# Optimization experiments

Measured on AMD Instinct MI355X. Metric: run time of the kernel, lower is better.

The kernel has to match this reference:

```python
import jax, jax.numpy as jnp
import numpy as np
from jax import lax

WINDOW_SIZE = 11
C1 = 0.01 ** 2
C2 = 0.03 ** 2


def make_window(window_size: int) -> jnp.ndarray:
    # scipy.ndimage.gaussian_filter(np.ones(ws), sigma) with mode='reflect'
    # preserves constant inputs exactly, so gauss_1d == ones(ws).
    # outer(ones, ones) / sum -> uniform box window of weight 1/ws^2.
    return jnp.full((window_size, window_size), 1.0 / (window_size * window_size), dtype=jnp.float32)


def setup_inputs() -> dict:
    key = jax.random.key(0)
    k1, k2 = jax.random.split(key)
    B, C, D, H, W = 1, 1, 64, 512, 512
    x = jax.random.uniform(k1, (B, C, D, H, W), dtype=jnp.float32)
    y = jax.random.uniform(k2, (B, C, D, H, W), dtype=jnp.float32)
    window = make_window(WINDOW_SIZE)
    return {"x": x, "y": y, "window": window}


def _windowed_sum(imgs, window):
    # imgs: [N,1,H,W]; window: [ws,ws]. 'same' cross-correlation (window is symmetric).
    ws = window.shape[0]
    pad = ws // 2
    w = window[None, None, :, :]  # [O=1, I=1, ws, ws]
    return lax.conv_general_dilated(
        imgs, w, window_strides=(1, 1), padding=[(pad, pad), (pad, pad)],
        dimension_numbers=("NCHW", "OIHW", "NCHW"))


def reference(x, y, window):
    B, C, D, H, W = x.shape
    # Fold depth into the conv batch dim: every depth slice is an independent 2D SSIM.
    xs = x.transpose(0, 2, 1, 3, 4).reshape(B * D, C, H, W)
    ys = y.transpose(0, 2, 1, 3, 4).reshape(B * D, C, H, W)
    # Single batched conv over [x, y, x^2, y^2, x*y]
    stacked = jnp.concatenate([xs, ys, xs * xs, ys * ys, xs * ys], axis=0)
    conv = _windowed_sum(stacked, window)
    mu_x, mu_y, e_x2, e_y2, e_xy = jnp.split(conv, 5, axis=0)
    mu_x_sq = mu_x * mu_x
    mu_y_sq = mu_y * mu_y
    mu_xy = mu_x * mu_y
    sigma_x_sq = e_x2 - mu_x_sq
    sigma_y_sq = e_y2 - mu_y_sq
    sigma_xy = e_xy - mu_xy
    ssim_map = ((2.0 * mu_xy + C1) * (2.0 * sigma_xy + C2)) / (
        (mu_x_sq + mu_y_sq + C1) * (sigma_x_sq + sigma_y_sq + C2))
    # Per-slice means averaged over slices == global mean (all slices same size).
    return 1.0 - ssim_map.mean()
```

## Files before the change

kernel.cpp:

```cpp
#include <hip/hip_runtime.h>


constexpr int IMG   = 512;
constexpr int RB    = 16;
constexpr int BANDS = IMG / RB;
constexpr int WPB   = 4;
constexpr int NBLK  = 64 * BANDS / WPB;
constexpr float K1 = 1.4641f;
constexpr float K2 = 13.1769f;

__device__ __forceinline__ float shr1(float v) {
  return __int_as_float(__builtin_amdgcn_update_dpp(
      0, __float_as_int(v), 0x138, 0xF, 0xF, true));
}
__device__ __forceinline__ float shl1(float v) {
  return __int_as_float(__builtin_amdgcn_update_dpp(
      0, __float_as_int(v), 0x130, 0xF, 0xF, true));
}

template <bool ATOMIC>
__global__ __launch_bounds__(256, 2) void ssim_main(const float* __restrict__ x,
                                                    const float* __restrict__ y,
                                                    float* __restrict__ out_ws) {
  __shared__ float wsum[WPB];

  const int tid  = threadIdx.x;
  const int lane = tid & 63;
  const int wid  = tid >> 6;

  const int bid  = blockIdx.x;
  const int xcd  = bid & 7;
  const int qq   = bid >> 3;
  const int z    = xcd * 8 + (qq >> 3);
  const int band = (qq & 7) * WPB + wid;
  const int o0   = band * RB;
  const int gs   = o0 - 5;

  const float* xs = x + (size_t)z * IMG * IMG + lane * 8;
  const float* ys = y + (size_t)z * IMG * IMG + lane * 8;

  float sX[8] = {}, sY[8] = {}, sXX[8] = {}, sYY[8] = {}, sXY[8] = {};
  float cxA[8], cyA[8], oxA[8], oyA[8];
  float cxB[8], cyB[8], oxB[8], oyB[8];
  float mcA = 0.f, mcB = 0.f, moA = 1.f, moB = 1.f;
  float acc = 0.f;

  auto LDraw = [&](int gr, float (&dx)[8], float (&dy)[8]) -> float {
    const int grc = gr < 0 ? 0 : (gr > IMG - 1 ? IMG - 1 : gr);
    const float* px = xs + (size_t)grc * IMG;
    const float* py = ys + (size_t)grc * IMG;
    const float4 a = *(const float4*)px;
    const float4 b = *(const float4*)(px + 4);
    const float4 c = *(const float4*)py;
    const float4 d = *(const float4*)(py + 4);
    dx[0] = a.x; dx[1] = a.y; dx[2] = a.z; dx[3] = a.w;
    dx[4] = b.x; dx[5] = b.y; dx[6] = b.z; dx[7] = b.w;
    dy[0] = c.x; dy[1] = c.y; dy[2] = c.z; dy[3] = c.w;
    dy[4] = d.x; dy[5] = d.y; dy[6] = d.z; dy[7] = d.w;
    return ((unsigned)gr < (unsigned)IMG) ? 1.f : 0.f;
  };

  auto consumeW = [&](const float (&cx)[8], const float (&cy)[8], float mc) {
#pragma unroll
    for (int j = 0; j < 8; ++j) {
      const float cxm = cx[j] * mc, cym = cy[j] * mc;
      sX[j] += cxm;
      sY[j] += cym;
      sXX[j] = fmaf(cx[j], cxm, sXX[j]);
      sYY[j] = fmaf(cy[j], cym, sYY[j]);
      sXY[j] = fmaf(cx[j], cym, sXY[j]);
    }
  };

  auto consumeS = [&](const float (&cx)[8], const float (&cy)[8], float mc,
                      const float (&ox)[8], const float (&oy)[8], float mo) {
#pragma unroll
    for (int j = 0; j < 8; ++j) {
      const float cxm = cx[j] * mc, cym = cy[j] * mc;
      const float oxm = ox[j] * mo, oym = oy[j] * mo;
      sX[j] += cxm - oxm;
      sY[j] += cym - oym;
      sXX[j] = fmaf(cx[j], cxm, fmaf(-ox[j], oxm, sXX[j]));
      sYY[j] = fmaf(cy[j], cym, fmaf(-oy[j], oym, sYY[j]));
      sXY[j] = fmaf(cx[j], cym, fmaf(-ox[j], oym, sXY[j]));
    }
  };

  auto hwin = [&](const float (&S)[8], float (&B)[8]) {
    const float vm5  = shr1(S[3]);
    const float vm4  = shr1(S[4]);
    const float vm3  = shr1(S[5]);
    const float vm2  = shr1(S[6]);
    const float vm1  = shr1(S[7]);
    const float vp8  = shl1(S[0]);
    const float vp9  = shl1(S[1]);
    const float vp10 = shl1(S[2]);
    const float vp11 = shl1(S[3]);
    const float vp12 = shl1(S[4]);
    float s = (((vm5 + vm4) + (vm3 + vm2)) + ((vm1 + S[0]) + (S[1] + S[2]))) +
              ((S[3] + S[4]) + S[5]);
    B[0] = s;
    s += S[6]  - vm5;  B[1] = s;
    s += S[7]  - vm4;  B[2] = s;
    s += vp8   - vm3;  B[3] = s;
    s += vp9   - vm2;  B[4] = s;
    s += vp10  - vm1;  B[5] = s;
    s += vp11  - S[0]; B[6] = s;
    s += vp12  - S[1]; B[7] = s;
  };

  auto outp = [&]() {
    float bX[8], bY[8], bXX[8], bYY[8], bXY[8];
    hwin(sX, bX); hwin(sY, bY); hwin(sXX, bXX); hwin(sYY, bYY); hwin(sXY, bXY);
#pragma unroll
    for (int j = 0; j < 8; ++j) {
      const float bx  = bX[j];
      const float by  = bY[j];
      const float bxy = bx * by;
      const float sq  = fmaf(bx, bx, by * by);
      const float n1  = fmaf(2.f, bxy, K1);
      const float n2  = fmaf(242.f, bXY[j], fmaf(-2.f, bxy, K2));
      const float d1  = sq + K1;
      const float d2  = fmaf(121.f, bXX[j] + bYY[j], K2 - sq);
      acc += (n1 * n2) * __builtin_amdgcn_rcpf(d1 * d2);
    }
  };

  mcA = LDraw(gs, cxA, cyA);
#pragma unroll
  for (int j = 0; j < 8; ++j) {
    oxA[j] = 0.f; oyA[j] = 0.f; oxB[j] = 0.f; oyB[j] = 0.f;
  }

#pragma unroll 1
  for (int i = 0; i < 10; i += 2) {
    mcB = LDraw(gs + i + 1, cxB, cyB);
    __builtin_amdgcn_sched_barrier(0);
    consumeW(cxA, cyA, mcA);
    mcA = LDraw(gs + i + 2, cxA, cyA);
    __builtin_amdgcn_sched_barrier(0);
    consumeW(cxB, cyB, mcB);
  }

#pragma unroll 1
  for (int i = 10; i < RB + 10; i += 2) {
    mcB = LDraw(gs + i + 1, cxB, cyB);
    moB = LDraw(gs + i - 10, oxB, oyB);
    __builtin_amdgcn_sched_barrier(0);
    consumeS(cxA, cyA, mcA, oxA, oyA, moA);
    outp();
    mcA = LDraw(gs + i + 2, cxA, cyA);
    moA = LDraw(gs + i - 9, oxA, oyA);
    __builtin_amdgcn_sched_barrier(0);
    consumeS(cxB, cyB, mcB, oxB, oyB, moB);
    outp();
  }

#pragma unroll
  for (int off = 32; off > 0; off >>= 1) acc += __shfl_down(acc, off, 64);
  if (lane == 0) wsum[wid] = acc;
  __syncthreads();
  if (tid == 0) {
    const float t = wsum[0] + wsum[1] + wsum[2] + wsum[3];
    if (ATOMIC) {
      atomicAdd(out_ws, t);
    } else {
      out_ws[bid] = t;
    }
  }
}

__global__ void ssim_finalize(const float* __restrict__ partials, int n,
                              float* __restrict__ out) {
  __shared__ float wsum[4];
  float acc = 0.f;
  for (int i = threadIdx.x; i < n; i += 256) acc += partials[i];
#pragma unroll
  for (int off = 32; off > 0; off >>= 1) acc += __shfl_down(acc, off, 64);
  if ((threadIdx.x & 63) == 0) wsum[threadIdx.x >> 6] = acc;
  __syncthreads();
  if (threadIdx.x == 0) {
    const float t = wsum[0] + wsum[1] + wsum[2] + wsum[3];
    out[0] = 1.0f - t * (1.0f / (64.0f * 512.0f * 512.0f));
  }
}

__global__ void ssim_zero(float* p) {
  if (threadIdx.x == 0) p[0] = 0.f;
}

__global__ void ssim_finalize_atomic(const float* __restrict__ accp,
                                     float* __restrict__ out) {
  if (threadIdx.x == 0)
    out[0] = 1.0f - accp[0] * (1.0f / (64.0f * 512.0f * 512.0f));
}

extern "C" void kernel_launch(void* const* d_in, const int* in_sizes, int n_in,
                              void* d_out, int out_size, void* d_ws, size_t ws_size,
                              hipStream_t stream) {
  const float* x = (const float*)d_in[0];
  const float* y = (const float*)d_in[1];
  float* out = (float*)d_out;

  dim3 grid(NBLK);
  dim3 block(256);

  if (ws_size >= (size_t)NBLK * sizeof(float)) {
    float* partials = (float*)d_ws;
    ssim_main<false><<<grid, block, 0, stream>>>(x, y, partials);
    ssim_finalize<<<1, 256, 0, stream>>>(partials, NBLK, out);
  } else {
    float* accp = (float*)d_ws;
    ssim_zero<<<1, 64, 0, stream>>>(accp);
    ssim_main<true><<<grid, block, 0, stream>>>(x, y, accp);
    ssim_finalize_atomic<<<1, 64, 0, stream>>>(accp, out);
  }
}
```

Measured before the change: 172.0 us.

## Stream rows into an LDS ring via async global_load_lds with one-wave blocks

Each block is now a single wavefront handling one 16-row band. Input rows (both the incoming and the outgoing row of the sliding window) are fetched with asynchronous global-to-LDS loads into a three-slot ring, and explicit vmcnt waits keep two rows in flight ahead of the computation. The goal is to hide global-load latency and free the registers that were used for the double-buffered rows. In exchange the kernel takes a 24KB LDS footprint per block, depends on hand-counted waitcnt values, and launches four times as many smaller blocks.

```diff
diff --git a/kernel.cpp b/kernel.cpp
--- a/kernel.cpp
+++ b/kernel.cpp
@@ -4,8 +4,7 @@
 constexpr int IMG   = 512;
 constexpr int RB    = 16;
 constexpr int BANDS = IMG / RB;
-constexpr int WPB   = 4;
-constexpr int NBLK  = 64 * BANDS / WPB;
+constexpr int NBLK  = 64 * BANDS;
 constexpr float K1 = 1.4641f;
 constexpr float K2 = 13.1769f;
 
@@ -18,72 +17,61 @@
       0, __float_as_int(v), 0x130, 0xF, 0xF, true));
 }
 
+__device__ __forceinline__ void gl16(const float* g, float* l) {
+  __builtin_amdgcn_global_load_lds(
+      (const __attribute__((address_space(1))) void*)g,
+      (__attribute__((address_space(3))) void*)l, 16, 0, 0);
+}
+
+#define VW(n) do {                                                             \
+    asm volatile("s_waitcnt vmcnt(%0)" :: "n"(n) : "memory");                  \
+    __builtin_amdgcn_sched_barrier(0);                                         \
+  } while (0)
+
 template <bool ATOMIC>
-__global__ __launch_bounds__(256, 2) void ssim_main(const float* __restrict__ x,
-                                                    const float* __restrict__ y,
-                                                    float* __restrict__ out_ws) {
-  __shared__ float wsum[WPB];
-
-  const int tid  = threadIdx.x;
-  const int lane = tid & 63;
-  const int wid  = tid >> 6;
-
+__global__ __launch_bounds__(64, 1) void ssim_main(const float* __restrict__ x,
+                                                   const float* __restrict__ y,
+                                                   float* __restrict__ out_ws) {
+  __shared__ float ring[3 * 2048];
+
+  const int lane = threadIdx.x;
   const int bid  = blockIdx.x;
   const int xcd  = bid & 7;
   const int qq   = bid >> 3;
-  const int z    = xcd * 8 + (qq >> 3);
-  const int band = (qq & 7) * WPB + wid;
+  const int z    = xcd * 8 + (qq >> 5);
+  const int band = qq & 31;
   const int o0   = band * RB;
   const int gs   = o0 - 5;
 
-  const float* xs = x + (size_t)z * IMG * IMG + lane * 8;
-  const float* ys = y + (size_t)z * IMG * IMG + lane * 8;
+  const float* xs = x + (size_t)z * IMG * IMG;
+  const float* ys = y + (size_t)z * IMG * IMG;
+  const int l4 = lane * 4;
+  const int lw = lane * 8;
 
   float sX[8] = {}, sY[8] = {}, sXX[8] = {}, sYY[8] = {}, sXY[8] = {};
-  float cxA[8], cyA[8], oxA[8], oyA[8];
-  float cxB[8], cyB[8], oxB[8], oyB[8];
-  float mcA = 0.f, mcB = 0.f, moA = 1.f, moB = 1.f;
   float acc = 0.f;
 
-  auto LDraw = [&](int gr, float (&dx)[8], float (&dy)[8]) -> float {
+  auto issue_c = [&](int slot) {
+    const int gr  = gs + slot;
     const int grc = gr < 0 ? 0 : (gr > IMG - 1 ? IMG - 1 : gr);
-    const float* px = xs + (size_t)grc * IMG;
-    const float* py = ys + (size_t)grc * IMG;
-    const float4 a = *(const float4*)px;
-    const float4 b = *(const float4*)(px + 4);
-    const float4 c = *(const float4*)py;
-    const float4 d = *(const float4*)(py + 4);
-    dx[0] = a.x; dx[1] = a.y; dx[2] = a.z; dx[3] = a.w;
-    dx[4] = b.x; dx[5] = b.y; dx[6] = b.z; dx[7] = b.w;
-    dy[0] = c.x; dy[1] = c.y; dy[2] = c.z; dy[3] = c.w;
-    dy[4] = d.x; dy[5] = d.y; dy[6] = d.z; dy[7] = d.w;
-    return ((unsigned)gr < (unsigned)IMG) ? 1.f : 0.f;
-  };
-
-  auto consumeW = [&](const float (&cx)[8], const float (&cy)[8], float mc) {
-#pragma unroll
-    for (int j = 0; j < 8; ++j) {
-      const float cxm = cx[j] * mc, cym = cy[j] * mc;
-      sX[j] += cxm;
-      sY[j] += cym;
-      sXX[j] = fmaf(cx[j], cxm, sXX[j]);
-      sYY[j] = fmaf(cy[j], cym, sYY[j]);
-      sXY[j] = fmaf(cx[j], cym, sXY[j]);
-    }
-  };
-
-  auto consumeS = [&](const float (&cx)[8], const float (&cy)[8], float mc,
-                      const float (&ox)[8], const float (&oy)[8], float mo) {
-#pragma unroll
-    for (int j = 0; j < 8; ++j) {
-      const float cxm = cx[j] * mc, cym = cy[j] * mc;
-      const float oxm = ox[j] * mo, oym = oy[j] * mo;
-      sX[j] += cxm - oxm;
-      sY[j] += cym - oym;
-      sXX[j] = fmaf(cx[j], cxm, fmaf(-ox[j], oxm, sXX[j]));
-      sYY[j] = fmaf(cy[j], cym, fmaf(-oy[j], oym, sYY[j]));
-      sXY[j] = fmaf(cx[j], cym, fmaf(-ox[j], oym, sXY[j]));
-    }
+    const int rb  = (slot % 3) * 2048;
+    const float* gx = xs + grc * IMG + l4;
+    const float* gy = ys + grc * IMG + l4;
+    gl16(gx,       &ring[rb]);
+    gl16(gx + 256, &ring[rb + 256]);
+    gl16(gy,       &ring[rb + 512]);
+    gl16(gy + 256, &ring[rb + 768]);
+  };
+  auto issue_o = [&](int slot) {
+    const int gr  = gs + slot - 11;
+    const int grc = gr < 0 ? 0 : (gr > IMG - 1 ? IMG - 1 : gr);
+    const int rb  = (slot % 3) * 2048;
+    const float* gx = xs + grc * IMG + l4;
+    const float* gy = ys + grc * IMG + l4;
+    gl16(gx,       &ring[rb + 1024]);
+    gl16(gx + 256, &ring[rb + 1280]);
+    gl16(gy,       &ring[rb + 1536]);
+    gl16(gy + 256, &ring[rb + 1792]);
   };
 
   auto hwin = [&](const float (&S)[8], float (&B)[8]) {
@@ -126,46 +114,88 @@
     }
   };
 
-  mcA = LDraw(gs, cxA, cyA);
-#pragma unroll
-  for (int j = 0; j < 8; ++j) {
-    oxA[j] = 0.f; oyA[j] = 0.f; oxB[j] = 0.f; oyB[j] = 0.f;
-  }
-
+  auto consumeW = [&](int slot) {
+    const int rb = (slot % 3) * 2048;
+    const float mc = ((unsigned)(gs + slot) < (unsigned)IMG) ? 1.f : 0.f;
+    const float4 a = *(const float4*)&ring[rb + lw];
+    const float4 b = *(const float4*)&ring[rb + lw + 4];
+    const float4 c = *(const float4*)&ring[rb + 512 + lw];
+    const float4 d = *(const float4*)&ring[rb + 512 + lw + 4];
+    const float cx[8] = {a.x, a.y, a.z, a.w, b.x, b.y, b.z, b.w};
+    const float cy[8] = {c.x, c.y, c.z, c.w, d.x, d.y, d.z, d.w};
+#pragma unroll
+    for (int j = 0; j < 8; ++j) {
+      const float cxm = cx[j] * mc, cym = cy[j] * mc;
+      sX[j] += cxm;
+      sY[j] += cym;
+      sXX[j] = fmaf(cx[j], cxm, sXX[j]);
+      sYY[j] = fmaf(cy[j], cym, sYY[j]);
+      sXY[j] = fmaf(cx[j], cym, sXY[j]);
+    }
+  };
+
+  auto consumeS = [&](int slot) {
+    const int rb = (slot % 3) * 2048;
+    const float mc = ((unsigned)(gs + slot) < (unsigned)IMG) ? 1.f : 0.f;
+    const float mo = (slot >= 11 && (gs + slot - 11) >= 0) ? 1.f : 0.f;
+    const float4 a = *(const float4*)&ring[rb + lw];
+    const float4 b = *(const float4*)&ring[rb + lw + 4];
+    const float4 c = *(const float4*)&ring[rb + 512 + lw];
+    const float4 d = *(const float4*)&ring[rb + 512 + lw + 4];
+    const float4 e = *(const float4*)&ring[rb + 1024 + lw];
+    const float4 f = *(const float4*)&ring[rb + 1024 + lw + 4];
+    const float4 g = *(const float4*)&ring[rb + 1536 + lw];
+    const float4 h = *(const float4*)&ring[rb + 1536 + lw + 4];
+    const float cx[8] = {a.x, a.y, a.z, a.w, b.x, b.y, b.z, b.w};
+    const float cy[8] = {c.x, c.y, c.z, c.w, d.x, d.y, d.z, d.w};
+    const float ox[8] = {e.x, e.y, e.z, e.w, f.x, f.y, f.z, f.w};
+    const float oy[8] = {g.x, g.y, g.z, g.w, h.x, h.y, h.z, h.w};
+#pragma unroll
+    for (int j = 0; j < 8; ++j) {
+      const float cxm = cx[j] * mc, cym = cy[j] * mc;
+      const float oxm = ox[j] * mo, oym = oy[j] * mo;
+      sX[j] += cxm - oxm;
+      sY[j] += cym - oym;
+      sXX[j] = fmaf(cx[j], cxm, fmaf(-ox[j], oxm, sXX[j]));
+      sYY[j] = fmaf(cy[j], cym, fmaf(-oy[j], oym, sYY[j]));
+      sXY[j] = fmaf(cx[j], cym, fmaf(-ox[j], oym, sXY[j]));
+    }
+    outp();
+  };
+
+  issue_c(0);
+  issue_c(1);
 #pragma unroll 1
-  for (int i = 0; i < 10; i += 2) {
-    mcB = LDraw(gs + i + 1, cxB, cyB);
-    __builtin_amdgcn_sched_barrier(0);
-    consumeW(cxA, cyA, mcA);
-    mcA = LDraw(gs + i + 2, cxA, cyA);
-    __builtin_amdgcn_sched_barrier(0);
-    consumeW(cxB, cyB, mcB);
-  }
-
+  for (int s = 0; s < 10; ++s) {
+    issue_c(s + 2);
+    VW(8);
+    consumeW(s);
+  }
+  issue_o(10);
+  issue_o(11);
+  issue_c(12);
+  issue_o(12);
+  VW(12);
+  consumeS(10);
 #pragma unroll 1
-  for (int i = 10; i < RB + 10; i += 2) {
-    mcB = LDraw(gs + i + 1, cxB, cyB);
-    moB = LDraw(gs + i - 10, oxB, oyB);
-    __builtin_amdgcn_sched_barrier(0);
-    consumeS(cxA, cyA, mcA, oxA, oyA, moA);
-    outp();
-    mcA = LDraw(gs + i + 2, cxA, cyA);
-    moA = LDraw(gs + i - 9, oxA, oyA);
-    __builtin_amdgcn_sched_barrier(0);
-    consumeS(cxB, cyB, mcB, oxB, oyB, moB);
-    outp();
-  }
+  for (int s = 11; s <= 23; ++s) {
+    issue_c(s + 2);
+    issue_o(s + 2);
+    VW(16);
+    consumeS(s);
+  }
+  VW(8);
+  consumeS(24);
+  VW(0);
+  consumeS(25);
 
 #pragma unroll
   for (int off = 32; off > 0; off >>= 1) acc += __shfl_down(acc, off, 64);
-  if (lane == 0) wsum[wid] = acc;
-  __syncthreads();
-  if (tid == 0) {
-    const float t = wsum[0] + wsum[1] + wsum[2] + wsum[3];
+  if (lane == 0) {
     if (ATOMIC) {
-      atomicAdd(out_ws, t);
+      atomicAdd(out_ws, acc);
     } else {
-      out_ws[bid] = t;
+      out_ws[bid] = acc;
     }
   }
 }
@@ -203,7 +233,7 @@
   float* out = (float*)d_out;
 
   dim3 grid(NBLK);
-  dim3 block(256);
+  dim3 block(64);
 
   if (ws_size >= (size_t)NBLK * sizeof(float)) {
     float* partials = (float*)d_ws;
```

After: 191.1 us. +11.1%, slower.

## Share row loads across warps via LDS ring with async global-to-LDS copies

Applied to the files above, without the earlier changes.

Each block now covers a 64-row group. Its four waves take overlapping 26-row windows of that group (16 output rows plus a 10-row halo) from a 16-slot LDS ring buffer that is filled with global_load_lds, one wave issuing each row four rows ahead. Before, every wave read its own halo rows and its outgoing rows straight from global memory, so global traffic was about 2.6x the image. Now each row is fetched once per block, and the rows leaving the window are re-read from LDS. The cost is a block-wide barrier on every row step and serialized staggering: each wave sits idle for the steps outside its window, which lowers compute utilization.

```diff
diff --git a/kernel.cpp b/kernel.cpp
--- a/kernel.cpp
+++ b/kernel.cpp
@@ -2,10 +2,10 @@
 
 
 constexpr int IMG   = 512;
-constexpr int RB    = 16;
-constexpr int BANDS = IMG / RB;
-constexpr int WPB   = 4;
-constexpr int NBLK  = 64 * BANDS / WPB;
+constexpr int GRB   = 64;
+constexpr int NROW  = GRB + 10;
+constexpr int NBLK  = 64 * (IMG / GRB);
+constexpr int SLOTS = 16;
 constexpr float K1 = 1.4641f;
 constexpr float K2 = 13.1769f;
 
@@ -16,13 +16,20 @@
 __device__ __forceinline__ float shl1(float v) {
   return __int_as_float(__builtin_amdgcn_update_dpp(
       0, __float_as_int(v), 0x130, 0xF, 0xF, true));
+}
+
+__device__ __forceinline__ void gl16(const float* g, float* l) {
+  __builtin_amdgcn_global_load_lds(
+      (const __attribute__((address_space(1))) void*)g,
+      (__attribute__((address_space(3))) void*)l, 16, 0, 0);
 }
 
 template <bool ATOMIC>
 __global__ __launch_bounds__(256, 2) void ssim_main(const float* __restrict__ x,
                                                     const float* __restrict__ y,
                                                     float* __restrict__ out_ws) {
-  __shared__ float wsum[WPB];
+  __shared__ float ring[SLOTS * 1024];
+  __shared__ float wsum[4];
 
   const int tid  = threadIdx.x;
   const int lane = tid & 63;
@@ -32,58 +39,27 @@
   const int xcd  = bid & 7;
   const int qq   = bid >> 3;
   const int z    = xcd * 8 + (qq >> 3);
-  const int band = (qq & 7) * WPB + wid;
-  const int o0   = band * RB;
-  const int gs   = o0 - 5;
-
-  const float* xs = x + (size_t)z * IMG * IMG + lane * 8;
-  const float* ys = y + (size_t)z * IMG * IMG + lane * 8;
+  const int g    = qq & 7;
+  const int R0   = g * GRB - 5;
+
+  const float* xs = x + (size_t)z * IMG * IMG;
+  const float* ys = y + (size_t)z * IMG * IMG;
+  const int l4 = lane * 4;
+  const int lw = lane * 8;
 
   float sX[8] = {}, sY[8] = {}, sXX[8] = {}, sYY[8] = {}, sXY[8] = {};
-  float cxA[8], cyA[8], oxA[8], oyA[8];
-  float cxB[8], cyB[8], oxB[8], oyB[8];
-  float mcA = 0.f, mcB = 0.f, moA = 1.f, moB = 1.f;
   float acc = 0.f;
 
-  auto LDraw = [&](int gr, float (&dx)[8], float (&dy)[8]) -> float {
-    const int grc = gr < 0 ? 0 : (gr > IMG - 1 ? IMG - 1 : gr);
-    const float* px = xs + (size_t)grc * IMG;
-    const float* py = ys + (size_t)grc * IMG;
-    const float4 a = *(const float4*)px;
-    const float4 b = *(const float4*)(px + 4);
-    const float4 c = *(const float4*)py;
-    const float4 d = *(const float4*)(py + 4);
-    dx[0] = a.x; dx[1] = a.y; dx[2] = a.z; dx[3] = a.w;
-    dx[4] = b.x; dx[5] = b.y; dx[6] = b.z; dx[7] = b.w;
-    dy[0] = c.x; dy[1] = c.y; dy[2] = c.z; dy[3] = c.w;
-    dy[4] = d.x; dy[5] = d.y; dy[6] = d.z; dy[7] = d.w;
-    return ((unsigned)gr < (unsigned)IMG) ? 1.f : 0.f;
-  };
-
-  auto consumeW = [&](const float (&cx)[8], const float (&cy)[8], float mc) {
-#pragma unroll
-    for (int j = 0; j < 8; ++j) {
-      const float cxm = cx[j] * mc, cym = cy[j] * mc;
-      sX[j] += cxm;
-      sY[j] += cym;
-      sXX[j] = fmaf(cx[j], cxm, sXX[j]);
-      sYY[j] = fmaf(cy[j], cym, sYY[j]);
-      sXY[j] = fmaf(cx[j], cym, sXY[j]);
-    }
-  };
-
-  auto consumeS = [&](const float (&cx)[8], const float (&cy)[8], float mc,
-                      const float (&ox)[8], const float (&oy)[8], float mo) {
-#pragma unroll
-    for (int j = 0; j < 8; ++j) {
-      const float cxm = cx[j] * mc, cym = cy[j] * mc;
-      const float oxm = ox[j] * mo, oym = oy[j] * mo;
-      sX[j] += cxm - oxm;
-      sY[j] += cym - oym;
-      sXX[j] = fmaf(cx[j], cxm, fmaf(-ox[j], oxm, sXX[j]));
-      sYY[j] = fmaf(cy[j], cym, fmaf(-oy[j], oym, sYY[j]));
-      sXY[j] = fmaf(cx[j], cym, fmaf(-ox[j], oym, sXY[j]));
-    }
+  auto issue_row = [&](int s) {
+    const int r   = R0 + s;
+    const int rc  = r < 0 ? 0 : (r > IMG - 1 ? IMG - 1 : r);
+    float* sb = &ring[(s & (SLOTS - 1)) * 1024];
+    const float* gx = xs + rc * IMG + l4;
+    const float* gy = ys + rc * IMG + l4;
+    gl16(gx,       sb);
+    gl16(gx + 256, sb + 256);
+    gl16(gy,       sb + 512);
+    gl16(gy + 256, sb + 768);
   };
 
   auto hwin = [&](const float (&S)[8], float (&B)[8]) {
@@ -126,34 +102,63 @@
     }
   };
 
-  mcA = LDraw(gs, cxA, cyA);
-#pragma unroll
-  for (int j = 0; j < 8; ++j) {
-    oxA[j] = 0.f; oyA[j] = 0.f; oxB[j] = 0.f; oyB[j] = 0.f;
-  }
+  issue_row(wid);
 
 #pragma unroll 1
-  for (int i = 0; i < 10; i += 2) {
-    mcB = LDraw(gs + i + 1, cxB, cyB);
+  for (int s = 0; s < NROW; ++s) {
+    if (wid == (s & 3)) {
+      asm volatile("s_waitcnt vmcnt(0)" ::: "memory");
+      __builtin_amdgcn_sched_barrier(0);
+    }
+    __builtin_amdgcn_s_barrier();
     __builtin_amdgcn_sched_barrier(0);
-    consumeW(cxA, cyA, mcA);
-    mcA = LDraw(gs + i + 2, cxA, cyA);
+
+    const int t = s - 16 * wid;
+    if (t >= 0 && t <= 25) {
+      const int r  = R0 + s;
+      const float mc = ((unsigned)r < (unsigned)IMG) ? 1.f : 0.f;
+      const float* sb = &ring[(s & (SLOTS - 1)) * 1024];
+      const float4 a = *(const float4*)(sb + lw);
+      const float4 b = *(const float4*)(sb + lw + 4);
+      const float4 c = *(const float4*)(sb + 512 + lw);
+      const float4 d = *(const float4*)(sb + 512 + lw + 4);
+      const float cx[8] = {a.x, a.y, a.z, a.w, b.x, b.y, b.z, b.w};
+      const float cy[8] = {c.x, c.y, c.z, c.w, d.x, d.y, d.z, d.w};
+      if (t < 11) {
+#pragma unroll
+        for (int j = 0; j < 8; ++j) {
+          const float cxm = cx[j] * mc, cym = cy[j] * mc;
+          sX[j] += cxm;
+          sY[j] += cym;
+          sXX[j] = fmaf(cx[j], cxm, sXX[j]);
+          sYY[j] = fmaf(cy[j], cym, sYY[j]);
+          sXY[j] = fmaf(cx[j], cym, sXY[j]);
+        }
+        if (t == 10) outp();
+      } else {
+        const float mo = ((unsigned)(r - 11) < (unsigned)IMG) ? 1.f : 0.f;
+        const float* so = &ring[((s - 11) & (SLOTS - 1)) * 1024];
+        const float4 e = *(const float4*)(so + lw);
+        const float4 f = *(const float4*)(so + lw + 4);
+        const float4 gg = *(const float4*)(so + 512 + lw);
+        const float4 h = *(const float4*)(so + 512 + lw + 4);
+        const float ox[8] = {e.x, e.y, e.z, e.w, f.x, f.y, f.z, f.w};
+        const float oy[8] = {gg.x, gg.y, gg.z, gg.w, h.x, h.y, h.z, h.w};
+#pragma unroll
+        for (int j = 0; j < 8; ++j) {
+          const float cxm = cx[j] * mc, cym = cy[j] * mc;
+          const float oxm = ox[j] * mo, oym = oy[j] * mo;
+          sX[j] += cxm - oxm;
+          sY[j] += cym - oym;
+          sXX[j] = fmaf(cx[j], cxm, fmaf(-ox[j], oxm, sXX[j]));
+          sYY[j] = fmaf(cy[j], cym, fmaf(-oy[j], oym, sYY[j]));
+          sXY[j] = fmaf(cx[j], cym, fmaf(-ox[j], oym, sXY[j]));
+        }
+        outp();
+      }
+    }
     __builtin_amdgcn_sched_barrier(0);
-    consumeW(cxB, cyB, mcB);
-  }
-
-#pragma unroll 1
-  for (int i = 10; i < RB + 10; i += 2) {
-    mcB = LDraw(gs + i + 1, cxB, cyB);
-    moB = LDraw(gs + i - 10, oxB, oyB);
-    __builtin_amdgcn_sched_barrier(0);
-    consumeS(cxA, cyA, mcA, oxA, oyA, moA);
-    outp();
-    mcA = LDraw(gs + i + 2, cxA, cyA);
-    moA = LDraw(gs + i - 9, oxA, oyA);
-    __builtin_amdgcn_sched_barrier(0);
-    consumeS(cxB, cyB, mcB, oxB, oyB, moB);
-    outp();
+    if (wid == (s & 3) && s + 4 < NROW) issue_row(s + 4);
   }
 
 #pragma unroll
```

After: 191.4 us. +11.3%, slower.
